# Optimization experiments

Measured on AMD Instinct MI355X. Metric: run time of the kernel, lower is better.

The kernel has to match this reference:

```python
import jax, jax.numpy as jnp
import numpy as np

HEADS = 16
HEAD_DIM = 64
EMB = HEADS * HEAD_DIM
MAX_REL = 512
B, L = 4, 1024


def _rel_indices(length_q, length_k):
    # Shaw-style clipped relative distance indices into the embeddings table
    dist = jnp.arange(length_k)[None, :] - jnp.arange(length_q)[:, None]
    return jnp.clip(dist, -MAX_REL, MAX_REL) + MAX_REL  # [Lq, Lk] in [0, 2*MAX_REL]


def setup_inputs() -> dict:
    key = jax.random.key(0)
    ks = jax.random.split(key, 16)
    d = {
        "query": jax.random.normal(ks[0], (B, L, EMB), jnp.float32),
        "key": jax.random.normal(ks[1], (B, L, EMB), jnp.float32),
        "value": jax.random.normal(ks[2], (B, L, EMB), jnp.float32),
        "mask": jnp.ones((B, 1, L, L), jnp.int32),
        # per-head Linear(head_dims, head_dims) weights stored torch-style [out, in]
        "Wq": jax.random.normal(ks[3], (HEAD_DIM, HEAD_DIM), jnp.float32) / np.sqrt(HEAD_DIM),
        "bq": jax.random.normal(ks[4], (HEAD_DIM,), jnp.float32) * 0.02,
        "Wk": jax.random.normal(ks[5], (HEAD_DIM, HEAD_DIM), jnp.float32) / np.sqrt(HEAD_DIM),
        "bk": jax.random.normal(ks[6], (HEAD_DIM,), jnp.float32) * 0.02,
        "Wv": jax.random.normal(ks[7], (HEAD_DIM, HEAD_DIM), jnp.float32) / np.sqrt(HEAD_DIM),
        "bv": jax.random.normal(ks[8], (HEAD_DIM,), jnp.float32) * 0.02,
        "Wfc": jax.random.normal(ks[9], (EMB, EMB), jnp.float32) / np.sqrt(EMB),
        "bfc": jax.random.normal(ks[10], (EMB,), jnp.float32) * 0.02,
        "rel_k_table": jax.random.normal(ks[11], (2 * MAX_REL + 1, HEAD_DIM), jnp.float32) * 0.02,
        "rel_v_table": jax.random.normal(ks[12], (2 * MAX_REL + 1, HEAD_DIM), jnp.float32) * 0.02,
    }
    return d


def reference(query, key, value, mask, Wq, bq, Wk, bk, Wv, bv, Wfc, bfc, rel_k_table, rel_v_table):
    b, lq, _ = query.shape
    lk = key.shape[1]
    # split heads then per-head linear projections (torch Linear: x @ W.T + b)
    q = query.reshape(b, lq, HEADS, HEAD_DIM) @ Wq.T + bq
    k = key.reshape(b, lk, HEADS, HEAD_DIM) @ Wk.T + bk
    v = value.reshape(b, lk, HEADS, HEAD_DIM) @ Wv.T + bv

    score = jnp.einsum('bqhd,bkhd->bhqk', q, k)  # [B,H,Lq,Lk]
    score = jnp.where(mask == 0, jnp.float32(-1e20), score)

    idx = _rel_indices(lq, lk)
    a_key = rel_k_table[idx]    # [Lq, Lk, D]
    a_val = rel_v_table[idx]    # [Lq, Lk, D]
    score = score + jnp.einsum('blhd,lrd->bhlr', q, a_key)

    attn = jax.nn.softmax(score / np.sqrt(HEAD_DIM), axis=-1)

    out = jnp.einsum('bhqv,bvhd->bqhd', attn, v)
    # original: einsum('brhl,hld->bhrd', attn[b,h,q,k], a_val[q,k,d]) -> [b,q,h,d]
    out = out + jnp.einsum('bhql,qld->bqhd', attn, a_val)
    out = out.reshape(b, lq, EMB)
    return out @ Wfc.T + bfc
```

## Files before the change

### kernel.cpp

```cpp
#include <hip/hip_runtime.h>
#include <hip/hip_bf16.h>
#include <hip/hip_fp16.h>

#define SEQ 1024
#define HEADS 16
#define HDIM 64
#define EMB 1024
#define TQ 16
#define KH 512
#define PBA_S 520
#define PBB_S 552
#define RELK_ROWS 1040
#define RELV_S 1064

typedef __bf16 bf16x8 __attribute__((ext_vector_type(8)));
typedef float floatx4 __attribute__((ext_vector_type(4)));

static __device__ __forceinline__ unsigned short f2bu(float f) {
    __bf16 h = (__bf16)f;
    return __builtin_bit_cast(unsigned short, h);
}
static __device__ __forceinline__ float b2f(unsigned short u) {
    unsigned v = ((unsigned)u) << 16;
    return __builtin_bit_cast(float, v);
}

__global__ __launch_bounds__(256) void sa_proj_kernel(
    const float* __restrict__ qin, const float* __restrict__ kin,
    const float* __restrict__ vin,
    const unsigned short* __restrict__ wqb, const unsigned short* __restrict__ wkb,
    const unsigned short* __restrict__ wvb,
    const float* __restrict__ bq, const float* __restrict__ bk,
    const float* __restrict__ bv_,
    unsigned short* __restrict__ qb, unsigned short* __restrict__ kb,
    unsigned short* __restrict__ vtb) {
    const int t = threadIdx.x;
    const int w = t >> 6, lane = t & 63;
    const int quad = lane >> 4, l16 = lane & 15;
    const int which = blockIdx.y;
    const int r0 = blockIdx.x * 16;
    const int bidx = r0 >> 10;
    const int l0 = r0 & 1023;
    const float* x = (which == 0) ? qin : (which == 1) ? kin : vin;
    const unsigned short* Wb = (which == 0) ? wqb : (which == 1) ? wkb : wvb;
    const float* bias = (which == 0) ? bq : (which == 1) ? bk : bv_;

    bf16x8 wf[4][2];
#pragma unroll
    for (int dt = 0; dt < 4; ++dt)
#pragma unroll
        for (int ks = 0; ks < 2; ++ks)
            wf[dt][ks] = *(const bf16x8*)(Wb + (size_t)(dt * 16 + l16) * 64 + ks * 32 + quad * 8);

    if (which < 2) {
        float biasd[4];
#pragma unroll
        for (int dt = 0; dt < 4; ++dt) biasd[dt] = bias[dt * 16 + l16];
        const float sc = (which == 0) ? 0.125f : 1.0f;
        unsigned short* dst = (which == 0) ? qb : kb;
        for (int hh = 0; hh < 4; ++hh) {
            const int h = w * 4 + hh;
            bf16x8 xf[2];
#pragma unroll
            for (int ks = 0; ks < 2; ++ks) {
                const float* xp = x + (size_t)(r0 + l16) * EMB + h * 64 + ks * 32 + quad * 8;
                float4 lo = *(const float4*)xp;
                float4 hi = *(const float4*)(xp + 4);
                unsigned short px[8];
                px[0] = f2bu(lo.x); px[1] = f2bu(lo.y); px[2] = f2bu(lo.z); px[3] = f2bu(lo.w);
                px[4] = f2bu(hi.x); px[5] = f2bu(hi.y); px[6] = f2bu(hi.z); px[7] = f2bu(hi.w);
                xf[ks] = *(bf16x8*)px;
            }
            floatx4 acc[4];
#pragma unroll
            for (int dt = 0; dt < 4; ++dt) acc[dt] = floatx4{0.f, 0.f, 0.f, 0.f};
#pragma unroll
            for (int dt = 0; dt < 4; ++dt)
#pragma unroll
                for (int ks = 0; ks < 2; ++ks)
                    acc[dt] = __builtin_amdgcn_mfma_f32_16x16x32_bf16(xf[ks], wf[dt][ks], acc[dt], 0, 0, 0);
            const int bh = bidx * HEADS + h;
#pragma unroll
            for (int dt = 0; dt < 4; ++dt)
#pragma unroll
                for (int i = 0; i < 4; ++i) {
                    const int lr = l0 + quad * 4 + i;
                    float val = (acc[dt][i] + biasd[dt]) * sc;
                    dst[((size_t)bh * SEQ + lr) * 64 + dt * 16 + l16] = f2bu(val);
                }
        }
    } else {
        float biasv[4][4];
#pragma unroll
        for (int dt = 0; dt < 4; ++dt)
#pragma unroll
            for (int i = 0; i < 4; ++i) biasv[dt][i] = bias[dt * 16 + quad * 4 + i];
        for (int hh = 0; hh < 4; ++hh) {
            const int h = w * 4 + hh;
            bf16x8 xf[2];
#pragma unroll
            for (int ks = 0; ks < 2; ++ks) {
                const float* xp = x + (size_t)(r0 + l16) * EMB + h * 64 + ks * 32 + quad * 8;
                float4 lo = *(const float4*)xp;
                float4 hi = *(const float4*)(xp + 4);
                unsigned short px[8];
                px[0] = f2bu(lo.x); px[1] = f2bu(lo.y); px[2] = f2bu(lo.z); px[3] = f2bu(lo.w);
                px[4] = f2bu(hi.x); px[5] = f2bu(hi.y); px[6] = f2bu(hi.z); px[7] = f2bu(hi.w);
                xf[ks] = *(bf16x8*)px;
            }
            floatx4 acc[4];
#pragma unroll
            for (int dt = 0; dt < 4; ++dt) acc[dt] = floatx4{0.f, 0.f, 0.f, 0.f};
#pragma unroll
            for (int dt = 0; dt < 4; ++dt)
#pragma unroll
                for (int ks = 0; ks < 2; ++ks)
                    acc[dt] = __builtin_amdgcn_mfma_f32_16x16x32_bf16(wf[dt][ks], xf[ks], acc[dt], 0, 0, 0);
            const int bh = bidx * HEADS + h;
#pragma unroll
            for (int dt = 0; dt < 4; ++dt)
#pragma unroll
                for (int i = 0; i < 4; ++i) {
                    const int d = dt * 16 + quad * 4 + i;
                    float val = acc[dt][i] + biasv[dt][i];
                    vtb[((size_t)bh * 64 + d) * SEQ + l0 + l16] = f2bu(val);
                }
        }
    }
}

#define NW (1024 * 1024)
#define NRK (RELK_ROWS * 64)
#define NRV (64 * RELV_S)
#define NWP (3 * 4096)
#define CONV_BLOCKS ((NW + NRK + NRV + NWP) / 256)
__global__ __launch_bounds__(256) void sa_prep_kernel(
    const float* __restrict__ Wfc, const float* __restrict__ relk,
    const float* __restrict__ relv,
    const float* __restrict__ Wq, const float* __restrict__ Wk,
    const float* __restrict__ Wv, const int* __restrict__ mask,
    unsigned short* __restrict__ wfcb, unsigned short* __restrict__ relkb,
    unsigned short* __restrict__ relvtb,
    unsigned short* __restrict__ wqb, unsigned short* __restrict__ wkb,
    unsigned short* __restrict__ wvb, unsigned* __restrict__ part) {
    const int bx = blockIdx.x;
    const int t = threadIdx.x;
    if (bx < CONV_BLOCKS) {
        int i = bx * 256 + t;
        if (i < NW) {
            wfcb[i] = f2bu(Wfc[i]);
        } else if (i < NW + NRK) {
            int j = i - NW;
            int r = j >> 6, d = j & 63;
            relkb[j] = (r <= 1024) ? f2bu(relk[r * 64 + d]) : 0;
        } else if (i < NW + NRK + NRV) {
            int j = i - NW - NRK;
            int d = j / RELV_S, c = j - d * RELV_S;
            relvtb[j] = (c <= 1024) ? f2bu(relv[c * 64 + d]) : 0;
        } else {
            int j = i - NW - NRK - NRV;
            int which = j >> 12, e = j & 4095;
            const float* src = (which == 0) ? Wq : (which == 1) ? Wk : Wv;
            unsigned short* dst = (which == 0) ? wqb : (which == 1) ? wkb : wvb;
            dst[e] = f2bu(src[e]);
        }
    } else {
        const int mb = bx - CONV_BLOCKS;
        const int b = mb >> 6, chunk = mb & 63;
        const int4* p = (const int4*)(mask + (size_t)b * (SEQ * SEQ) + chunk * 16384);
        int ok = 1;
#pragma unroll
        for (int i = 0; i < 16; ++i) {
            int4 v = p[t + i * 256];
            ok &= (v.x != 0 && v.y != 0 && v.z != 0 && v.w != 0) ? 1 : 0;
        }
        unsigned long long bal = __ballot(ok);
        __shared__ unsigned wok[4];
        if ((t & 63) == 0) wok[t >> 6] = (bal == ~0ull) ? 1u : 0u;
        __syncthreads();
        if (t == 0)
            part[b * 64 + chunk] = (wok[0] & wok[1] & wok[2] & wok[3]) ? 0xFFFFFFFFu : 0u;
    }
}

__global__ void sa_maskred2(const unsigned* __restrict__ part, unsigned* __restrict__ flags) {
    int t = threadIdx.x;
    if (t < 4) {
        unsigned f = 0xFFFFFFFFu;
        for (int i = 0; i < 64; ++i) f &= part[t * 64 + i];
        flags[t] = f;
    }
}

__global__ __launch_bounds__(512, 8) void sa_attn_kernel(
    const unsigned short* __restrict__ qb, const unsigned short* __restrict__ kb,
    const unsigned short* __restrict__ vtb, const int* __restrict__ mask,
    const unsigned short* __restrict__ relkb, const unsigned short* __restrict__ relvtb,
    const unsigned* __restrict__ flags, __half* __restrict__ Opart,
    float2* __restrict__ ms) {
    __shared__ __align__(16) unsigned short PbA[TQ * PBA_S];
    __shared__ __align__(16) unsigned short PbB[TQ * PBB_S];
    __shared__ float Ored[TQ * 64];
    __shared__ float wred[4][128];
    __shared__ float lowS[TQ], highS[TQ];

    const int tid = threadIdx.x;
    const int w = tid >> 6, lane = tid & 63;
    const int quad = lane >> 4, l16 = lane & 15;
    const int bid = blockIdx.x;
    const int hf = bid & 1;
    const int qt = (bid >> 1) & 63;
    const int bh = bid >> 7;
    const int q0 = qt * TQ;
    const int k0 = hf * KH;
    const int b = bh >> 4;
    const bool mfull = (flags[b] == 0xFFFFFFFFu);

    const int cmin = min(512, max(-512, k0 - (q0 + 15))) + 512;
    const int cmax = min(512, max(-512, k0 + 511 - q0)) + 512;
    const int rsb = cmin & ~15;
    const int cb0 = cmin & ~7;

    bf16x8 aq[2];
    {
        const unsigned short* qrow = qb + ((size_t)bh * SEQ + q0 + l16) * 64;
        aq[0] = *(const bf16x8*)(qrow + quad * 8);
        aq[1] = *(const bf16x8*)(qrow + 32 + quad * 8);
    }

    {
        const int rt_lo = cmin >> 4, rt_hi = cmax >> 4;
        for (int rt = rt_lo + w; rt <= rt_hi; rt += 8) {
            floatx4 racc = {0.f, 0.f, 0.f, 0.f};
#pragma unroll
            for (int ks = 0; ks < 2; ++ks) {
                bf16x8 bf = *(const bf16x8*)(relkb + (size_t)(rt * 16 + l16) * 64 + ks * 32 + quad * 8);
                racc = __builtin_amdgcn_mfma_f32_16x16x32_bf16(aq[ks], bf, racc, 0, 0, 0);
            }
            const int rcol = rt * 16 + l16;
            if (rcol <= cmax) {
#pragma unroll
                for (int i = 0; i < 4; ++i)
                    PbB[(quad * 4 + i) * PBB_S + (rcol - rsb)] = f2bu(racc[i]);
            }
        }
    }
    __syncthreads();

    const int kbase = k0 + w * 64;
    floatx4 acc[4];
#pragma unroll
    for (int tt = 0; tt < 4; ++tt) acc[tt] = floatx4{0.f, 0.f, 0.f, 0.f};
#pragma unroll
    for (int tt = 0; tt < 4; ++tt) {
#pragma unroll
        for (int ks = 0; ks < 2; ++ks) {
            bf16x8 bf = *(const bf16x8*)(
                kb + ((size_t)bh * SEQ + kbase + tt * 16 + l16) * 64 + ks * 32 + quad * 8);
            acc[tt] = __builtin_amdgcn_mfma_f32_16x16x32_bf16(aq[ks], bf, acc[tt], 0, 0, 0);
        }
    }
    float rmax[4] = {-3.0e38f, -3.0e38f, -3.0e38f, -3.0e38f};
    if (mfull) {
#pragma unroll
        for (int tt = 0; tt < 4; ++tt) {
            const int k = kbase + tt * 16 + l16;
#pragma unroll
            for (int i = 0; i < 4; ++i) {
                const int row = quad * 4 + i;
                const int q = q0 + row;
                int r = min(512, max(-512, k - q)) + 512;
                float s = acc[tt][i] + b2f(PbB[row * PBB_S + (r - rsb)]);
                acc[tt][i] = s;
                rmax[i] = fmaxf(rmax[i], s);
            }
        }
    } else {
#pragma unroll
        for (int tt = 0; tt < 4; ++tt) {
            const int k = kbase + tt * 16 + l16;
#pragma unroll
            for (int i = 0; i < 4; ++i) {
                const int row = quad * 4 + i;
                const int q = q0 + row;
                int r = min(512, max(-512, k - q)) + 512;
                float s = acc[tt][i] + b2f(PbB[row * PBB_S + (r - rsb)]);
                int m = mask[(size_t)b * (SEQ * SEQ) + (size_t)q * SEQ + k];
                s = (m == 0) ? -1e20f : s;
                acc[tt][i] = s;
                rmax[i] = fmaxf(rmax[i], s);
            }
        }
    }
#pragma unroll
    for (int i = 0; i < 4; ++i) {
#pragma unroll
        for (int o = 1; o < 16; o <<= 1) rmax[i] = fmaxf(rmax[i], __shfl_xor(rmax[i], o));
    }
    if (l16 == 0) {
#pragma unroll
        for (int i = 0; i < 4; ++i) wred[0][(quad * 4 + i) * 8 + w] = rmax[i];
    }
    __syncthreads();

    for (int g = tid; g < TQ * (PBB_S / 8); g += 512) {
        int row = g / (PBB_S / 8), j = g - row * (PBB_S / 8);
        *(uint4*)&PbB[row * PBB_S + j * 8] = make_uint4(0u, 0u, 0u, 0u);
    }
    float mx[4];
#pragma unroll
    for (int i = 0; i < 4; ++i) {
        const int row = quad * 4 + i;
        float4 a = *(float4*)&wred[0][row * 8];
        float4 c = *(float4*)&wred[0][row * 8 + 4];
        mx[i] = fmaxf(fmaxf(fmaxf(a.x, a.y), fmaxf(a.z, a.w)),
                      fmaxf(fmaxf(c.x, c.y), fmaxf(c.z, c.w)));
    }
    __syncthreads();

    float ssum[4] = {0.f, 0.f, 0.f, 0.f};
    float slow[4] = {0.f, 0.f, 0.f, 0.f};
    float shigh[4] = {0.f, 0.f, 0.f, 0.f};
#pragma unroll
    for (int tt = 0; tt < 4; ++tt) {
        const int k = kbase + tt * 16 + l16;
#pragma unroll
        for (int i = 0; i < 4; ++i) {
            const int row = quad * 4 + i;
            const int q = q0 + row;
            float p = __expf(acc[tt][i] - mx[i]);
            ssum[i] += p;
            const int dist = k - q;
            slow[i] += (dist <= -512) ? p : 0.f;
            shigh[i] += (dist >= 512) ? p : 0.f;
            unsigned short pv = f2bu(p);
            PbA[row * PBA_S + (k - k0)] = pv;
            const int c = dist + 512;
            if ((unsigned)(c - 1) < 1023u) PbB[row * PBB_S + (c - cb0)] = pv;
        }
    }
#pragma unroll
    for (int i = 0; i < 4; ++i) {
#pragma unroll
        for (int o = 1; o < 16; o <<= 1) {
            ssum[i] += __shfl_xor(ssum[i], o);
            slow[i] += __shfl_xor(slow[i], o);
            shigh[i] += __shfl_xor(shigh[i], o);
        }
    }
    if (l16 == 0) {
#pragma unroll
        for (int i = 0; i < 4; ++i) {
            const int row = quad * 4 + i;
            wred[1][row * 8 + w] = ssum[i];
            wred[2][row * 8 + w] = slow[i];
            wred[3][row * 8 + w] = shigh[i];
        }
    }
    __syncthreads();
    if (tid < TQ) {
        float m = wred[0][tid * 8];
        float s = 0.f, lo = 0.f, hi = 0.f;
#pragma unroll
        for (int j = 0; j < 8; ++j) {
            m = fmaxf(m, wred[0][tid * 8 + j]);
            s += wred[1][tid * 8 + j];
            lo += wred[2][tid * 8 + j];
            hi += wred[3][tid * 8 + j];
        }
        lowS[tid] = lo;
        highS[tid] = hi;
        const int R = bh * SEQ + q0 + tid;
        ms[(size_t)R * 2 + hf] = make_float2(m, s);
    }
    __syncthreads();

    const int d0 = (w & 3) * 16;
    const int kg = w >> 2;
    floatx4 accA = {0.f, 0.f, 0.f, 0.f};
    floatx4 accB = {0.f, 0.f, 0.f, 0.f};
    const unsigned short* vbase = vtb + ((size_t)bh * 64 + d0 + l16) * SEQ + k0;
    const unsigned short* rbase = relvtb + (size_t)(d0 + l16) * RELV_S;
    for (int ks = kg; ks < 16; ks += 2) {
        const int co = ks * 32 + quad * 8;
        bf16x8 ap = *(const bf16x8*)&PbA[l16 * PBA_S + co];
        bf16x8 bv = *(const bf16x8*)(vbase + co);
        accA = __builtin_amdgcn_mfma_f32_16x16x32_bf16(ap, bv, accA, 0, 0, 0);
    }
    const int nksB = ((cmax - cb0) >> 5) + 1;
    for (int ks = kg; ks < nksB; ks += 2) {
        const int co = ks * 32 + quad * 8;
        bf16x8 ar = *(const bf16x8*)&PbB[l16 * PBB_S + co];
        bf16x8 br = *(const bf16x8*)(rbase + cb0 + co);
        accB = __builtin_amdgcn_mfma_f32_16x16x32_bf16(ar, br, accB, 0, 0, 0);
    }
    if (w >= 4) {
#pragma unroll
        for (int i = 0; i < 4; ++i)
            Ored[(quad * 4 + i) * 64 + d0 + l16] = accA[i] + accB[i];
    }
    __syncthreads();
    if (w < 4) {
        const float rv0 = b2f(rbase[0]);
        const float rv1 = b2f(rbase[1024]);
#pragma unroll
        for (int i = 0; i < 4; ++i) {
            const int row = quad * 4 + i;
            const int R = bh * SEQ + q0 + row;
            float val = accA[i] + accB[i] + Ored[row * 64 + d0 + l16] +
                        lowS[row] * rv0 + highS[row] * rv1;
            Opart[((size_t)R * 2 + hf) * 64 + d0 + l16] = __float2half(val);
        }
    }
}

__global__ __launch_bounds__(256) void sa_combine_kernel(
    const __half* __restrict__ Opart, const float2* __restrict__ ms,
    unsigned short* __restrict__ aob) {
    const int tid = threadIdx.x;
    const int R = blockIdx.x * 4 + (tid >> 6);
    const int d = tid & 63;
    float2 s0 = ms[(size_t)R * 2 + 0];
    float2 s1 = ms[(size_t)R * 2 + 1];
    float m = fmaxf(s0.x, s1.x);
    float a0 = __expf(s0.x - m), a1 = __expf(s1.x - m);
    float inv = 1.f / (s0.y * a0 + s1.y * a1);
    float O0 = __half2float(Opart[((size_t)R * 2 + 0) * 64 + d]);
    float O1 = __half2float(Opart[((size_t)R * 2 + 1) * 64 + d]);
    float val = (O0 * a0 + O1 * a1) * inv;
    const int bh = R >> 10, q = R & 1023, b = bh >> 4, h = bh & 15;
    aob[((size_t)b * SEQ + q) * EMB + h * 64 + d] = f2bu(val);
}

__global__ __launch_bounds__(256, 2) void sa_fc_kernel(
    const unsigned short* __restrict__ A, const unsigned short* __restrict__ W,
    const float* __restrict__ bias, float* __restrict__ out) {
    const int t = threadIdx.x;
    const int w = t >> 6, lane = t & 63;
    const int quad = lane >> 4, l16 = lane & 15;
    const int mw = blockIdx.x * 64 + (w & 1) * 32;
    const int nw = blockIdx.y * 256 + (w >> 1) * 128;

    floatx4 acc[2][8];
#pragma unroll
    for (int mt = 0; mt < 2; ++mt)
#pragma unroll
        for (int j = 0; j < 8; ++j) acc[mt][j] = floatx4{0.f, 0.f, 0.f, 0.f};
    float bj[8];
#pragma unroll
    for (int j = 0; j < 8; ++j) bj[j] = bias[nw + j * 16 + l16];

    for (int ks = 0; ks < 32; ++ks) {
        const int co = ks * 32 + quad * 8;
        bf16x8 af0 = *(const bf16x8*)(A + (size_t)(mw + l16) * EMB + co);
        bf16x8 af1 = *(const bf16x8*)(A + (size_t)(mw + 16 + l16) * EMB + co);
#pragma unroll
        for (int j = 0; j < 8; ++j) {
            bf16x8 bf = *(const bf16x8*)(W + (size_t)(nw + j * 16 + l16) * EMB + co);
            acc[0][j] = __builtin_amdgcn_mfma_f32_16x16x32_bf16(af0, bf, acc[0][j], 0, 0, 0);
            acc[1][j] = __builtin_amdgcn_mfma_f32_16x16x32_bf16(af1, bf, acc[1][j], 0, 0, 0);
        }
    }
#pragma unroll
    for (int mt = 0; mt < 2; ++mt)
#pragma unroll
        for (int j = 0; j < 8; ++j) {
            const int col = nw + j * 16 + l16;
#pragma unroll
            for (int i = 0; i < 4; ++i) {
                const size_t row = mw + mt * 16 + quad * 4 + i;
                out[row * EMB + col] = acc[mt][j][i] + bj[j];
            }
        }
}

extern "C" void kernel_launch(void* const* d_in, const int* in_sizes, int n_in,
                              void* d_out, int out_size, void* d_ws, size_t ws_size,
                              hipStream_t stream) {
    const float* query = (const float*)d_in[0];
    const float* key = (const float*)d_in[1];
    const float* value = (const float*)d_in[2];
    const int* mask = (const int*)d_in[3];
    const float* Wq = (const float*)d_in[4];
    const float* bq = (const float*)d_in[5];
    const float* Wk = (const float*)d_in[6];
    const float* bk = (const float*)d_in[7];
    const float* Wv = (const float*)d_in[8];
    const float* bv = (const float*)d_in[9];
    const float* Wfc = (const float*)d_in[10];
    const float* bfc = (const float*)d_in[11];
    const float* relk = (const float*)d_in[12];
    const float* relv = (const float*)d_in[13];
    float* out = (float*)d_out;

    char* base = (char*)d_ws;
    const size_t MB = (size_t)1 << 20;
    unsigned short* qb = (unsigned short*)(base + 0 * MB);
    unsigned short* kb = (unsigned short*)(base + 8 * MB);
    unsigned short* vtb = (unsigned short*)(base + 16 * MB);
    unsigned short* aob = (unsigned short*)(base + 24 * MB);
    unsigned short* wfcb = (unsigned short*)(base + 32 * MB);
    unsigned short* relkb = (unsigned short*)(base + 34 * MB);
    unsigned short* relvtb = (unsigned short*)(base + 34 * MB + 262144);
    unsigned short* wqb = (unsigned short*)(base + 34 * MB + 524288);
    unsigned short* wkb = (unsigned short*)(base + 34 * MB + 532480);
    unsigned short* wvb = (unsigned short*)(base + 34 * MB + 540672);
    unsigned* flags = (unsigned*)(base + 34 * MB + 548864);
    unsigned* part = (unsigned*)(base + 34 * MB + 552960);
    float2* ms = (float2*)(base + 35 * MB);
    __half* Opart = (__half*)(base + 36 * MB);

    sa_prep_kernel<<<CONV_BLOCKS + 256, 256, 0, stream>>>(
        Wfc, relk, relv, Wq, Wk, Wv, mask, wfcb, relkb, relvtb, wqb, wkb, wvb, part);
    sa_proj_kernel<<<dim3(256, 3), 256, 0, stream>>>(
        query, key, value, wqb, wkb, wvb, bq, bk, bv, qb, kb, vtb);
    sa_maskred2<<<1, 64, 0, stream>>>(part, flags);
    sa_attn_kernel<<<64 * 64 * 2, 512, 0, stream>>>(
        qb, kb, vtb, mask, relkb, relvtb, flags, Opart, ms);
    sa_combine_kernel<<<(4 * HEADS * SEQ) / 4, 256, 0, stream>>>(Opart, ms, aob);
    sa_fc_kernel<<<dim3(64, 4), 256, 0, stream>>>(aob, wfcb, bfc, out);
}
```

Baseline: 412.0 us.

## Retile attention to 32-query tiles over key quarters and spread projection over more blocks

The attention kernel now processes 32 query rows per block and splits the key range into four 256-wide quarters instead of two halves. Each wave handles both 16-row sub-tiles, so every K and rel-K fragment load feeds two MFMAs. The relative-value tail sums are merged, and the per-wave cross-reduction through Ored is dropped. The combine kernel merges four partials instead of two, and the projection kernel uses one head per wave across four times as many blocks to raise parallelism. The trade-off is more partial outputs to write and combine, and a compacted workspace layout where aob now aliases the q buffer.

```diff
diff --git a/kernel.cpp b/kernel.cpp
--- a/kernel.cpp
+++ b/kernel.cpp
@@ -6,10 +6,10 @@
 #define HEADS 16
 #define HDIM 64
 #define EMB 1024
-#define TQ 16
-#define KH 512
-#define PBA_S 520
-#define PBB_S 552
+#define TQ 32
+#define KQ 256
+#define PBA_S 264
+#define PBB_S 328
 #define RELK_ROWS 1040
 #define RELV_S 1064
 
@@ -38,7 +38,9 @@
     const int w = t >> 6, lane = t & 63;
     const int quad = lane >> 4, l16 = lane & 15;
     const int which = blockIdx.y;
-    const int r0 = blockIdx.x * 16;
+    const int bx = blockIdx.x;
+    const int r0 = (bx >> 2) * 16;
+    const int h = (bx & 3) * 4 + w;
     const int bidx = r0 >> 10;
     const int l0 = r0 & 1023;
     const float* x = (which == 0) ? qin : (which == 1) ? kin : vin;
@@ -52,80 +54,63 @@
         for (int ks = 0; ks < 2; ++ks)
             wf[dt][ks] = *(const bf16x8*)(Wb + (size_t)(dt * 16 + l16) * 64 + ks * 32 + quad * 8);
 
+    bf16x8 xf[2];
+#pragma unroll
+    for (int ks = 0; ks < 2; ++ks) {
+        const float* xp = x + (size_t)(r0 + l16) * EMB + h * 64 + ks * 32 + quad * 8;
+        float4 lo = *(const float4*)xp;
+        float4 hi = *(const float4*)(xp + 4);
+        unsigned short px[8];
+        px[0] = f2bu(lo.x); px[1] = f2bu(lo.y); px[2] = f2bu(lo.z); px[3] = f2bu(lo.w);
+        px[4] = f2bu(hi.x); px[5] = f2bu(hi.y); px[6] = f2bu(hi.z); px[7] = f2bu(hi.w);
+        xf[ks] = *(bf16x8*)px;
+    }
+    const int bh = bidx * HEADS + h;
+
     if (which < 2) {
         float biasd[4];
 #pragma unroll
         for (int dt = 0; dt < 4; ++dt) biasd[dt] = bias[dt * 16 + l16];
         const float sc = (which == 0) ? 0.125f : 1.0f;
         unsigned short* dst = (which == 0) ? qb : kb;
-        for (int hh = 0; hh < 4; ++hh) {
-            const int h = w * 4 + hh;
-            bf16x8 xf[2];
-#pragma unroll
-            for (int ks = 0; ks < 2; ++ks) {
-                const float* xp = x + (size_t)(r0 + l16) * EMB + h * 64 + ks * 32 + quad * 8;
-                float4 lo = *(const float4*)xp;
-                float4 hi = *(const float4*)(xp + 4);
-                unsigned short px[8];
-                px[0] = f2bu(lo.x); px[1] = f2bu(lo.y); px[2] = f2bu(lo.z); px[3] = f2bu(lo.w);
-                px[4] = f2bu(hi.x); px[5] = f2bu(hi.y); px[6] = f2bu(hi.z); px[7] = f2bu(hi.w);
-                xf[ks] = *(bf16x8*)px;
-            }
-            floatx4 acc[4];
-#pragma unroll
-            for (int dt = 0; dt < 4; ++dt) acc[dt] = floatx4{0.f, 0.f, 0.f, 0.f};
-#pragma unroll
-            for (int dt = 0; dt < 4; ++dt)
-#pragma unroll
-                for (int ks = 0; ks < 2; ++ks)
-                    acc[dt] = __builtin_amdgcn_mfma_f32_16x16x32_bf16(xf[ks], wf[dt][ks], acc[dt], 0, 0, 0);
-            const int bh = bidx * HEADS + h;
-#pragma unroll
-            for (int dt = 0; dt < 4; ++dt)
-#pragma unroll
-                for (int i = 0; i < 4; ++i) {
-                    const int lr = l0 + quad * 4 + i;
-                    float val = (acc[dt][i] + biasd[dt]) * sc;
-                    dst[((size_t)bh * SEQ + lr) * 64 + dt * 16 + l16] = f2bu(val);
-                }
-        }
+        floatx4 acc[4];
+#pragma unroll
+        for (int dt = 0; dt < 4; ++dt) acc[dt] = floatx4{0.f, 0.f, 0.f, 0.f};
+#pragma unroll
+        for (int dt = 0; dt < 4; ++dt)
+#pragma unroll
+            for (int ks = 0; ks < 2; ++ks)
+                acc[dt] = __builtin_amdgcn_mfma_f32_16x16x32_bf16(xf[ks], wf[dt][ks], acc[dt], 0, 0, 0);
+#pragma unroll
+        for (int dt = 0; dt < 4; ++dt)
+#pragma unroll
+            for (int i = 0; i < 4; ++i) {
+                const int lr = l0 + quad * 4 + i;
+                float val = (acc[dt][i] + biasd[dt]) * sc;
+                dst[((size_t)bh * SEQ + lr) * 64 + dt * 16 + l16] = f2bu(val);
+            }
     } else {
         float biasv[4][4];
 #pragma unroll
         for (int dt = 0; dt < 4; ++dt)
 #pragma unroll
             for (int i = 0; i < 4; ++i) biasv[dt][i] = bias[dt * 16 + quad * 4 + i];
-        for (int hh = 0; hh < 4; ++hh) {
-            const int h = w * 4 + hh;
-            bf16x8 xf[2];
-#pragma unroll
-            for (int ks = 0; ks < 2; ++ks) {
-                const float* xp = x + (size_t)(r0 + l16) * EMB + h * 64 + ks * 32 + quad * 8;
-                float4 lo = *(const float4*)xp;
-                float4 hi = *(const float4*)(xp + 4);
-                unsigned short px[8];
-                px[0] = f2bu(lo.x); px[1] = f2bu(lo.y); px[2] = f2bu(lo.z); px[3] = f2bu(lo.w);
-                px[4] = f2bu(hi.x); px[5] = f2bu(hi.y); px[6] = f2bu(hi.z); px[7] = f2bu(hi.w);
-                xf[ks] = *(bf16x8*)px;
-            }
-            floatx4 acc[4];
-#pragma unroll
-            for (int dt = 0; dt < 4; ++dt) acc[dt] = floatx4{0.f, 0.f, 0.f, 0.f};
-#pragma unroll
-            for (int dt = 0; dt < 4; ++dt)
-#pragma unroll
-                for (int ks = 0; ks < 2; ++ks)
-                    acc[dt] = __builtin_amdgcn_mfma_f32_16x16x32_bf16(wf[dt][ks], xf[ks], acc[dt], 0, 0, 0);
-            const int bh = bidx * HEADS + h;
-#pragma unroll
-            for (int dt = 0; dt < 4; ++dt)
-#pragma unroll
-                for (int i = 0; i < 4; ++i) {
-                    const int d = dt * 16 + quad * 4 + i;
-                    float val = acc[dt][i] + biasv[dt][i];
-                    vtb[((size_t)bh * 64 + d) * SEQ + l0 + l16] = f2bu(val);
-                }
-        }
+        floatx4 acc[4];
+#pragma unroll
+        for (int dt = 0; dt < 4; ++dt) acc[dt] = floatx4{0.f, 0.f, 0.f, 0.f};
+#pragma unroll
+        for (int dt = 0; dt < 4; ++dt)
+#pragma unroll
+            for (int ks = 0; ks < 2; ++ks)
+                acc[dt] = __builtin_amdgcn_mfma_f32_16x16x32_bf16(wf[dt][ks], xf[ks], acc[dt], 0, 0, 0);
+#pragma unroll
+        for (int dt = 0; dt < 4; ++dt)
+#pragma unroll
+            for (int i = 0; i < 4; ++i) {
+                const int d = dt * 16 + quad * 4 + i;
+                float val = acc[dt][i] + biasv[dt][i];
+                vtb[((size_t)bh * 64 + d) * SEQ + l0 + l16] = f2bu(val);
+            }
     }
 }
 
@@ -200,216 +185,233 @@
     float2* __restrict__ ms) {
     __shared__ __align__(16) unsigned short PbA[TQ * PBA_S];
     __shared__ __align__(16) unsigned short PbB[TQ * PBB_S];
-    __shared__ float Ored[TQ * 64];
-    __shared__ float wred[4][128];
-    __shared__ float lowS[TQ], highS[TQ];
+    __shared__ float wred[3][TQ * 8];
 
     const int tid = threadIdx.x;
     const int w = tid >> 6, lane = tid & 63;
     const int quad = lane >> 4, l16 = lane & 15;
     const int bid = blockIdx.x;
-    const int hf = bid & 1;
-    const int qt = (bid >> 1) & 63;
+    const int quarter = bid & 3;
+    const int qt = (bid >> 2) & 31;
     const int bh = bid >> 7;
     const int q0 = qt * TQ;
-    const int k0 = hf * KH;
+    const int k0 = quarter * KQ;
     const int b = bh >> 4;
     const bool mfull = (flags[b] == 0xFFFFFFFFu);
 
-    const int cmin = min(512, max(-512, k0 - (q0 + 15))) + 512;
-    const int cmax = min(512, max(-512, k0 + 511 - q0)) + 512;
+    const int cmin = min(512, max(-512, k0 - (q0 + 31))) + 512;
+    const int cmax = min(512, max(-512, k0 + 255 - q0)) + 512;
     const int rsb = cmin & ~15;
     const int cb0 = cmin & ~7;
 
-    bf16x8 aq[2];
+    bf16x8 aq[2][2];
+#pragma unroll
+    for (int rt = 0; rt < 2; ++rt) {
+        const unsigned short* qrow = qb + ((size_t)bh * SEQ + q0 + rt * 16 + l16) * 64;
+        aq[rt][0] = *(const bf16x8*)(qrow + quad * 8);
+        aq[rt][1] = *(const bf16x8*)(qrow + 32 + quad * 8);
+    }
+
     {
-        const unsigned short* qrow = qb + ((size_t)bh * SEQ + q0 + l16) * 64;
-        aq[0] = *(const bf16x8*)(qrow + quad * 8);
-        aq[1] = *(const bf16x8*)(qrow + 32 + quad * 8);
-    }
-
-    {
-        const int rt_lo = cmin >> 4, rt_hi = cmax >> 4;
-        for (int rt = rt_lo + w; rt <= rt_hi; rt += 8) {
-            floatx4 racc = {0.f, 0.f, 0.f, 0.f};
-#pragma unroll
-            for (int ks = 0; ks < 2; ++ks) {
-                bf16x8 bf = *(const bf16x8*)(relkb + (size_t)(rt * 16 + l16) * 64 + ks * 32 + quad * 8);
-                racc = __builtin_amdgcn_mfma_f32_16x16x32_bf16(aq[ks], bf, racc, 0, 0, 0);
-            }
-            const int rcol = rt * 16 + l16;
+        const int ct_lo = cmin >> 4, ct_hi = cmax >> 4;
+        for (int ct = ct_lo + w; ct <= ct_hi; ct += 8) {
+            bf16x8 bf0 = *(const bf16x8*)(relkb + (size_t)(ct * 16 + l16) * 64 + quad * 8);
+            bf16x8 bf1 = *(const bf16x8*)(relkb + (size_t)(ct * 16 + l16) * 64 + 32 + quad * 8);
+            floatx4 r0 = {0.f, 0.f, 0.f, 0.f}, r1 = {0.f, 0.f, 0.f, 0.f};
+            r0 = __builtin_amdgcn_mfma_f32_16x16x32_bf16(aq[0][0], bf0, r0, 0, 0, 0);
+            r0 = __builtin_amdgcn_mfma_f32_16x16x32_bf16(aq[0][1], bf1, r0, 0, 0, 0);
+            r1 = __builtin_amdgcn_mfma_f32_16x16x32_bf16(aq[1][0], bf0, r1, 0, 0, 0);
+            r1 = __builtin_amdgcn_mfma_f32_16x16x32_bf16(aq[1][1], bf1, r1, 0, 0, 0);
+            const int rcol = ct * 16 + l16;
             if (rcol <= cmax) {
 #pragma unroll
-                for (int i = 0; i < 4; ++i)
-                    PbB[(quad * 4 + i) * PBB_S + (rcol - rsb)] = f2bu(racc[i]);
+                for (int i = 0; i < 4; ++i) {
+                    PbB[(quad * 4 + i) * PBB_S + (rcol - rsb)] = f2bu(r0[i]);
+                    PbB[(16 + quad * 4 + i) * PBB_S + (rcol - rsb)] = f2bu(r1[i]);
+                }
             }
         }
     }
     __syncthreads();
 
-    const int kbase = k0 + w * 64;
-    floatx4 acc[4];
-#pragma unroll
-    for (int tt = 0; tt < 4; ++tt) acc[tt] = floatx4{0.f, 0.f, 0.f, 0.f};
-#pragma unroll
-    for (int tt = 0; tt < 4; ++tt) {
-#pragma unroll
-        for (int ks = 0; ks < 2; ++ks) {
-            bf16x8 bf = *(const bf16x8*)(
-                kb + ((size_t)bh * SEQ + kbase + tt * 16 + l16) * 64 + ks * 32 + quad * 8);
-            acc[tt] = __builtin_amdgcn_mfma_f32_16x16x32_bf16(aq[ks], bf, acc[tt], 0, 0, 0);
-        }
-    }
-    float rmax[4] = {-3.0e38f, -3.0e38f, -3.0e38f, -3.0e38f};
+    const int kc = w;
+    floatx4 acc[2][2];
+#pragma unroll
+    for (int rt = 0; rt < 2; ++rt)
+#pragma unroll
+        for (int tt = 0; tt < 2; ++tt) acc[rt][tt] = floatx4{0.f, 0.f, 0.f, 0.f};
+#pragma unroll
+    for (int tt = 0; tt < 2; ++tt) {
+        const unsigned short* krow = kb + ((size_t)bh * SEQ + k0 + kc * 32 + tt * 16 + l16) * 64;
+        bf16x8 kf0 = *(const bf16x8*)(krow + quad * 8);
+        bf16x8 kf1 = *(const bf16x8*)(krow + 32 + quad * 8);
+        acc[0][tt] = __builtin_amdgcn_mfma_f32_16x16x32_bf16(aq[0][0], kf0, acc[0][tt], 0, 0, 0);
+        acc[0][tt] = __builtin_amdgcn_mfma_f32_16x16x32_bf16(aq[0][1], kf1, acc[0][tt], 0, 0, 0);
+        acc[1][tt] = __builtin_amdgcn_mfma_f32_16x16x32_bf16(aq[1][0], kf0, acc[1][tt], 0, 0, 0);
+        acc[1][tt] = __builtin_amdgcn_mfma_f32_16x16x32_bf16(aq[1][1], kf1, acc[1][tt], 0, 0, 0);
+    }
+    float rmax[2][4];
+#pragma unroll
+    for (int rt = 0; rt < 2; ++rt)
+#pragma unroll
+        for (int i = 0; i < 4; ++i) rmax[rt][i] = -3.0e38f;
     if (mfull) {
 #pragma unroll
-        for (int tt = 0; tt < 4; ++tt) {
-            const int k = kbase + tt * 16 + l16;
-#pragma unroll
-            for (int i = 0; i < 4; ++i) {
-                const int row = quad * 4 + i;
-                const int q = q0 + row;
-                int r = min(512, max(-512, k - q)) + 512;
-                float s = acc[tt][i] + b2f(PbB[row * PBB_S + (r - rsb)]);
-                acc[tt][i] = s;
-                rmax[i] = fmaxf(rmax[i], s);
-            }
-        }
+        for (int rt = 0; rt < 2; ++rt)
+#pragma unroll
+            for (int tt = 0; tt < 2; ++tt) {
+                const int k = k0 + kc * 32 + tt * 16 + l16;
+#pragma unroll
+                for (int i = 0; i < 4; ++i) {
+                    const int row = rt * 16 + quad * 4 + i;
+                    const int q = q0 + row;
+                    int r = min(512, max(-512, k - q)) + 512;
+                    float s = acc[rt][tt][i] + b2f(PbB[row * PBB_S + (r - rsb)]);
+                    acc[rt][tt][i] = s;
+                    rmax[rt][i] = fmaxf(rmax[rt][i], s);
+                }
+            }
     } else {
 #pragma unroll
-        for (int tt = 0; tt < 4; ++tt) {
-            const int k = kbase + tt * 16 + l16;
-#pragma unroll
-            for (int i = 0; i < 4; ++i) {
-                const int row = quad * 4 + i;
-                const int q = q0 + row;
-                int r = min(512, max(-512, k - q)) + 512;
-                float s = acc[tt][i] + b2f(PbB[row * PBB_S + (r - rsb)]);
-                int m = mask[(size_t)b * (SEQ * SEQ) + (size_t)q * SEQ + k];
-                s = (m == 0) ? -1e20f : s;
-                acc[tt][i] = s;
-                rmax[i] = fmaxf(rmax[i], s);
-            }
-        }
-    }
-#pragma unroll
-    for (int i = 0; i < 4; ++i) {
-#pragma unroll
-        for (int o = 1; o < 16; o <<= 1) rmax[i] = fmaxf(rmax[i], __shfl_xor(rmax[i], o));
-    }
+        for (int rt = 0; rt < 2; ++rt)
+#pragma unroll
+            for (int tt = 0; tt < 2; ++tt) {
+                const int k = k0 + kc * 32 + tt * 16 + l16;
+#pragma unroll
+                for (int i = 0; i < 4; ++i) {
+                    const int row = rt * 16 + quad * 4 + i;
+                    const int q = q0 + row;
+                    int r = min(512, max(-512, k - q)) + 512;
+                    float s = acc[rt][tt][i] + b2f(PbB[row * PBB_S + (r - rsb)]);
+                    int m = mask[(size_t)b * (SEQ * SEQ) + (size_t)q * SEQ + k];
+                    s = (m == 0) ? -1e20f : s;
+                    acc[rt][tt][i] = s;
+                    rmax[rt][i] = fmaxf(rmax[rt][i], s);
+                }
+            }
+    }
+#pragma unroll
+    for (int rt = 0; rt < 2; ++rt)
+#pragma unroll
+        for (int i = 0; i < 4; ++i) {
+#pragma unroll
+            for (int o = 1; o < 16; o <<= 1)
+                rmax[rt][i] = fmaxf(rmax[rt][i], __shfl_xor(rmax[rt][i], o));
+        }
     if (l16 == 0) {
 #pragma unroll
-        for (int i = 0; i < 4; ++i) wred[0][(quad * 4 + i) * 8 + w] = rmax[i];
+        for (int rt = 0; rt < 2; ++rt)
+#pragma unroll
+            for (int i = 0; i < 4; ++i)
+                wred[0][(rt * 16 + quad * 4 + i) * 8 + kc] = rmax[rt][i];
     }
     __syncthreads();
 
+    if (tid < TQ) {
+        float m = wred[0][tid * 8];
+#pragma unroll
+        for (int j = 1; j < 8; ++j) m = fmaxf(m, wred[0][tid * 8 + j]);
+        wred[0][tid * 8] = m;
+    }
     for (int g = tid; g < TQ * (PBB_S / 8); g += 512) {
         int row = g / (PBB_S / 8), j = g - row * (PBB_S / 8);
         *(uint4*)&PbB[row * PBB_S + j * 8] = make_uint4(0u, 0u, 0u, 0u);
     }
-    float mx[4];
-#pragma unroll
-    for (int i = 0; i < 4; ++i) {
-        const int row = quad * 4 + i;
-        float4 a = *(float4*)&wred[0][row * 8];
-        float4 c = *(float4*)&wred[0][row * 8 + 4];
-        mx[i] = fmaxf(fmaxf(fmaxf(a.x, a.y), fmaxf(a.z, a.w)),
-                      fmaxf(fmaxf(c.x, c.y), fmaxf(c.z, c.w)));
-    }
     __syncthreads();
 
-    float ssum[4] = {0.f, 0.f, 0.f, 0.f};
-    float slow[4] = {0.f, 0.f, 0.f, 0.f};
-    float shigh[4] = {0.f, 0.f, 0.f, 0.f};
-#pragma unroll
-    for (int tt = 0; tt < 4; ++tt) {
-        const int k = kbase + tt * 16 + l16;
+    float mxr[2][4];
+#pragma unroll
+    for (int rt = 0; rt < 2; ++rt)
+#pragma unroll
+        for (int i = 0; i < 4; ++i)
+            mxr[rt][i] = wred[0][(rt * 16 + quad * 4 + i) * 8];
+    float ssum[2][4] = {{0.f, 0.f, 0.f, 0.f}, {0.f, 0.f, 0.f, 0.f}};
+    float tail[2][4] = {{0.f, 0.f, 0.f, 0.f}, {0.f, 0.f, 0.f, 0.f}};
+#pragma unroll
+    for (int rt = 0; rt < 2; ++rt)
+#pragma unroll
+        for (int tt = 0; tt < 2; ++tt) {
+            const int k = k0 + kc * 32 + tt * 16 + l16;
+#pragma unroll
+            for (int i = 0; i < 4; ++i) {
+                const int row = rt * 16 + quad * 4 + i;
+                const int q = q0 + row;
+                float p = __expf(acc[rt][tt][i] - mxr[rt][i]);
+                ssum[rt][i] += p;
+                const int c = k - q + 512;
+                const bool interior = ((unsigned)(c - 1) < 1023u);
+                tail[rt][i] += interior ? 0.f : p;
+                unsigned short pv = f2bu(p);
+                PbA[row * PBA_S + (k - k0)] = pv;
+                if (interior) PbB[row * PBB_S + (c - cb0)] = pv;
+            }
+        }
+#pragma unroll
+    for (int rt = 0; rt < 2; ++rt)
 #pragma unroll
         for (int i = 0; i < 4; ++i) {
-            const int row = quad * 4 + i;
-            const int q = q0 + row;
-            float p = __expf(acc[tt][i] - mx[i]);
-            ssum[i] += p;
-            const int dist = k - q;
-            slow[i] += (dist <= -512) ? p : 0.f;
-            shigh[i] += (dist >= 512) ? p : 0.f;
-            unsigned short pv = f2bu(p);
-            PbA[row * PBA_S + (k - k0)] = pv;
-            const int c = dist + 512;
-            if ((unsigned)(c - 1) < 1023u) PbB[row * PBB_S + (c - cb0)] = pv;
-        }
-    }
-#pragma unroll
-    for (int i = 0; i < 4; ++i) {
-#pragma unroll
-        for (int o = 1; o < 16; o <<= 1) {
-            ssum[i] += __shfl_xor(ssum[i], o);
-            slow[i] += __shfl_xor(slow[i], o);
-            shigh[i] += __shfl_xor(shigh[i], o);
-        }
-    }
+#pragma unroll
+            for (int o = 1; o < 16; o <<= 1) {
+                ssum[rt][i] += __shfl_xor(ssum[rt][i], o);
+                tail[rt][i] += __shfl_xor(tail[rt][i], o);
+            }
+        }
     if (l16 == 0) {
 #pragma unroll
-        for (int i = 0; i < 4; ++i) {
-            const int row = quad * 4 + i;
-            wred[1][row * 8 + w] = ssum[i];
-            wred[2][row * 8 + w] = slow[i];
-            wred[3][row * 8 + w] = shigh[i];
-        }
+        for (int rt = 0; rt < 2; ++rt)
+#pragma unroll
+            for (int i = 0; i < 4; ++i) {
+                const int row = rt * 16 + quad * 4 + i;
+                wred[1][row * 8 + kc] = ssum[rt][i];
+                wred[2][row * 8 + kc] = tail[rt][i];
+            }
     }
     __syncthreads();
     if (tid < TQ) {
-        float m = wred[0][tid * 8];
-        float s = 0.f, lo = 0.f, hi = 0.f;
+        float s = 0.f, t = 0.f;
 #pragma unroll
         for (int j = 0; j < 8; ++j) {
-            m = fmaxf(m, wred[0][tid * 8 + j]);
             s += wred[1][tid * 8 + j];
-            lo += wred[2][tid * 8 + j];
-            hi += wred[3][tid * 8 + j];
-        }
-        lowS[tid] = lo;
-        highS[tid] = hi;
-        const int R = bh * SEQ + q0 + tid;
-        ms[(size_t)R * 2 + hf] = make_float2(m, s);
+            t += wred[2][tid * 8 + j];
+        }
+        const int q = q0 + tid;
+        wred[0][tid * 8 + 1] = (q >= k0 + 512) ? t : 0.f;
+        wred[0][tid * 8 + 2] = (q <= k0 - 257) ? t : 0.f;
+        const int R = bh * SEQ + q;
+        ms[(size_t)R * 4 + quarter] = make_float2(wred[0][tid * 8], s);
     }
     __syncthreads();
 
-    const int d0 = (w & 3) * 16;
-    const int kg = w >> 2;
-    floatx4 accA = {0.f, 0.f, 0.f, 0.f};
-    floatx4 accB = {0.f, 0.f, 0.f, 0.f};
-    const unsigned short* vbase = vtb + ((size_t)bh * 64 + d0 + l16) * SEQ + k0;
-    const unsigned short* rbase = relvtb + (size_t)(d0 + l16) * RELV_S;
-    for (int ks = kg; ks < 16; ks += 2) {
-        const int co = ks * 32 + quad * 8;
-        bf16x8 ap = *(const bf16x8*)&PbA[l16 * PBA_S + co];
-        bf16x8 bv = *(const bf16x8*)(vbase + co);
-        accA = __builtin_amdgcn_mfma_f32_16x16x32_bf16(ap, bv, accA, 0, 0, 0);
-    }
-    const int nksB = ((cmax - cb0) >> 5) + 1;
-    for (int ks = kg; ks < nksB; ks += 2) {
-        const int co = ks * 32 + quad * 8;
-        bf16x8 ar = *(const bf16x8*)&PbB[l16 * PBB_S + co];
-        bf16x8 br = *(const bf16x8*)(rbase + cb0 + co);
-        accB = __builtin_amdgcn_mfma_f32_16x16x32_bf16(ar, br, accB, 0, 0, 0);
-    }
-    if (w >= 4) {
-#pragma unroll
-        for (int i = 0; i < 4; ++i)
-            Ored[(quad * 4 + i) * 64 + d0 + l16] = accA[i] + accB[i];
-    }
-    __syncthreads();
-    if (w < 4) {
+    {
+        const int rt = w & 1;
+        const int dq = w >> 1;
+        floatx4 accA = {0.f, 0.f, 0.f, 0.f};
+        floatx4 accB = {0.f, 0.f, 0.f, 0.f};
+        const unsigned short* vbase = vtb + ((size_t)bh * 64 + dq * 16 + l16) * SEQ + k0;
+        const unsigned short* rbase = relvtb + (size_t)(dq * 16 + l16) * RELV_S;
+#pragma unroll
+        for (int it = 0; it < 8; ++it) {
+            const int co = it * 32 + quad * 8;
+            bf16x8 ap = *(const bf16x8*)&PbA[(rt * 16 + l16) * PBA_S + co];
+            bf16x8 bv = *(const bf16x8*)(vbase + co);
+            accA = __builtin_amdgcn_mfma_f32_16x16x32_bf16(ap, bv, accA, 0, 0, 0);
+        }
+        const int nksB = ((cmax - cb0) >> 5) + 1;
+        for (int ks = 0; ks < nksB; ++ks) {
+            const int co = ks * 32 + quad * 8;
+            bf16x8 ar = *(const bf16x8*)&PbB[(rt * 16 + l16) * PBB_S + co];
+            bf16x8 br = *(const bf16x8*)(rbase + cb0 + co);
+            accB = __builtin_amdgcn_mfma_f32_16x16x32_bf16(ar, br, accB, 0, 0, 0);
+        }
         const float rv0 = b2f(rbase[0]);
         const float rv1 = b2f(rbase[1024]);
 #pragma unroll
         for (int i = 0; i < 4; ++i) {
-            const int row = quad * 4 + i;
+            const int row = rt * 16 + quad * 4 + i;
             const int R = bh * SEQ + q0 + row;
-            float val = accA[i] + accB[i] + Ored[row * 64 + d0 + l16] +
-                        lowS[row] * rv0 + highS[row] * rv1;
-            Opart[((size_t)R * 2 + hf) * 64 + d0 + l16] = __float2half(val);
+            float val = accA[i] + accB[i] +
+                        wred[0][row * 8 + 1] * rv0 + wred[0][row * 8 + 2] * rv1;
+            Opart[((size_t)R * 4 + quarter) * 64 + dq * 16 + l16] = __float2half(val);
         }
     }
 }
@@ -420,14 +422,22 @@
     const int tid = threadIdx.x;
     const int R = blockIdx.x * 4 + (tid >> 6);
     const int d = tid & 63;
-    float2 s0 = ms[(size_t)R * 2 + 0];
-    float2 s1 = ms[(size_t)R * 2 + 1];
-    float m = fmaxf(s0.x, s1.x);
-    float a0 = __expf(s0.x - m), a1 = __expf(s1.x - m);
-    float inv = 1.f / (s0.y * a0 + s1.y * a1);
-    float O0 = __half2float(Opart[((size_t)R * 2 + 0) * 64 + d]);
-    float O1 = __half2float(Opart[((size_t)R * 2 + 1) * 64 + d]);
-    float val = (O0 * a0 + O1 * a1) * inv;
+    float2 s[4];
+#pragma unroll
+    for (int j = 0; j < 4; ++j) s[j] = ms[(size_t)R * 4 + j];
+    float m = fmaxf(fmaxf(s[0].x, s[1].x), fmaxf(s[2].x, s[3].x));
+    float a[4], denom = 0.f;
+#pragma unroll
+    for (int j = 0; j < 4; ++j) {
+        a[j] = __expf(s[j].x - m);
+        denom += s[j].y * a[j];
+    }
+    float inv = 1.f / denom;
+    float val = 0.f;
+#pragma unroll
+    for (int j = 0; j < 4; ++j)
+        val += __half2float(Opart[((size_t)R * 4 + j) * 64 + d]) * a[j];
+    val *= inv;
     const int bh = R >> 10, q = R & 1023, b = bh >> 4, h = bh & 15;
     aob[((size_t)b * SEQ + q) * EMB + h * 64 + d] = f2bu(val);
 }
@@ -496,26 +506,26 @@
     char* base = (char*)d_ws;
     const size_t MB = (size_t)1 << 20;
     unsigned short* qb = (unsigned short*)(base + 0 * MB);
+    unsigned short* aob = qb;
     unsigned short* kb = (unsigned short*)(base + 8 * MB);
     unsigned short* vtb = (unsigned short*)(base + 16 * MB);
-    unsigned short* aob = (unsigned short*)(base + 24 * MB);
-    unsigned short* wfcb = (unsigned short*)(base + 32 * MB);
-    unsigned short* relkb = (unsigned short*)(base + 34 * MB);
-    unsigned short* relvtb = (unsigned short*)(base + 34 * MB + 262144);
-    unsigned short* wqb = (unsigned short*)(base + 34 * MB + 524288);
-    unsigned short* wkb = (unsigned short*)(base + 34 * MB + 532480);
-    unsigned short* wvb = (unsigned short*)(base + 34 * MB + 540672);
-    unsigned* flags = (unsigned*)(base + 34 * MB + 548864);
-    unsigned* part = (unsigned*)(base + 34 * MB + 552960);
-    float2* ms = (float2*)(base + 35 * MB);
-    __half* Opart = (__half*)(base + 36 * MB);
+    unsigned short* wfcb = (unsigned short*)(base + 24 * MB);
+    unsigned short* relkb = (unsigned short*)(base + 26 * MB);
+    unsigned short* relvtb = (unsigned short*)(base + 26 * MB + 163840);
+    unsigned short* wqb = (unsigned short*)(base + 26 * MB + 327680);
+    unsigned short* wkb = (unsigned short*)(base + 26 * MB + 335872);
+    unsigned short* wvb = (unsigned short*)(base + 26 * MB + 344064);
+    unsigned* flags = (unsigned*)(base + 26 * MB + 360448);
+    unsigned* part = (unsigned*)(base + 26 * MB + 364544);
+    float2* ms = (float2*)(base + 27 * MB);
+    __half* Opart = (__half*)(base + 29 * MB);
 
     sa_prep_kernel<<<CONV_BLOCKS + 256, 256, 0, stream>>>(
         Wfc, relk, relv, Wq, Wk, Wv, mask, wfcb, relkb, relvtb, wqb, wkb, wvb, part);
-    sa_proj_kernel<<<dim3(256, 3), 256, 0, stream>>>(
+    sa_proj_kernel<<<dim3(1024, 3), 256, 0, stream>>>(
         query, key, value, wqb, wkb, wvb, bq, bk, bv, qb, kb, vtb);
     sa_maskred2<<<1, 64, 0, stream>>>(part, flags);
-    sa_attn_kernel<<<64 * 64 * 2, 512, 0, stream>>>(
+    sa_attn_kernel<<<64 * 32 * 4, 512, 0, stream>>>(
         qb, kb, vtb, mask, relkb, relvtb, flags, Opart, ms);
     sa_combine_kernel<<<(4 * HEADS * SEQ) / 4, 256, 0, stream>>>(Opart, ms, aob);
     sa_fc_kernel<<<dim3(64, 4), 256, 0, stream>>>(aob, wfcb, bfc, out);
```

Result: faster. 402.2 us (-2.4%).
